# Kernel optimization log

Measured on AMD Instinct MI355X. Metric: run time of the kernel, lower is better.

The kernel has to match this reference:

```python
import jax, jax.numpy as jnp
import numpy as np

N_HEADS = 16
SCALE = 8.0  # sqrt(inner_dim // n_heads) = sqrt(64), scale='inv_sqrt'


def setup_inputs() -> dict:
    key = jax.random.key(0)
    k1, k2, k3, k4 = jax.random.split(key, 4)
    b, n, d_model, inner = 8, 2048, 1024, 1024
    x = jax.random.normal(k1, (b, n, d_model), dtype=jnp.float32)
    Wqkv = jax.random.normal(k2, (3 * inner, d_model), dtype=jnp.float32) * (1.0 / np.sqrt(d_model))
    Wproj = jax.random.normal(k3, (d_model, inner), dtype=jnp.float32) * (1.0 / np.sqrt(inner))
    bproj = jax.random.normal(k4, (d_model,), dtype=jnp.float32) * 0.01
    return {"x": x, "Wqkv": Wqkv, "Wproj": Wproj, "bproj": bproj}


def reference(x, Wqkv, Wproj, bproj):
    b, n, _ = x.shape
    qkv = jnp.einsum('bnm,fm->bnf', x, Wqkv)          # [b, n, 3*inner]
    qkv = qkv.reshape(b, n, N_HEADS, -1)              # [b, n, h, 3*dh] (einops 'b n (h d)')
    dh = qkv.shape[3] // 3
    q, k, v = qkv[..., :dh], qkv[..., dh:2 * dh], qkv[..., 2 * dh:]
    # Faithful to source: q @ k.transpose(-1,-2) on [b,n,h,dh] -> scores over HEADS, [b,n,h,h]
    scores = jnp.einsum('bnhd,bngd->bnhg', q, k) / SCALE
    attn = jax.nn.softmax(scores, axis=-1)            # softmax over last head axis
    out = jnp.einsum('bnhg,bngd->bnhd', attn, v)      # [b, n, h, dh]
    out = out.reshape(b, n, -1)                       # [b, n, inner]
    return jnp.einsum('bni,mi->bnm', out, Wproj) + bproj
```

## Files before the change

### kernel.cpp

```cpp
#include <hip/hip_runtime.h>
#include <stdint.h>

typedef __bf16 bf16_t;
typedef __bf16 bf16x8 __attribute__((ext_vector_type(8)));
typedef float f32x4 __attribute__((ext_vector_type(4)));

__device__ __forceinline__ void gload_lds16(const void* g, void* l) {
  __builtin_amdgcn_global_load_lds(
      (const __attribute__((address_space(1))) uint32_t*)g,
      (__attribute__((address_space(3))) uint32_t*)l, 16, 0, 0);
}

__global__ void cast3_f32_bf16(const float* __restrict__ a, bf16_t* __restrict__ ao, int n4a,
                               const float* __restrict__ b, bf16_t* __restrict__ bo, int n4b,
                               const float* __restrict__ c, bf16_t* __restrict__ co, int n4c) {
  int i = blockIdx.x * blockDim.x + threadIdx.x;
  int stride = gridDim.x * blockDim.x;
  int total = n4a + n4b + n4c;
  for (int idx = i; idx < total; idx += stride) {
    const float* src; bf16_t* dst; int j = idx;
    if (j < n4a) { src = a; dst = ao; }
    else if ((j -= n4a) < n4b) { src = b; dst = bo; }
    else { j -= n4b; src = c; dst = co; }
    float4 v = reinterpret_cast<const float4*>(src)[j];
    union { bf16_t b[4]; uint2 u; } pk;
    pk.b[0] = (bf16_t)v.x; pk.b[1] = (bf16_t)v.y;
    pk.b[2] = (bf16_t)v.z; pk.b[3] = (bf16_t)v.w;
    reinterpret_cast<uint2*>(dst)[j] = pk.u;
  }
}

template <bool BF16_OUT>
__global__ __launch_bounds__(512, 2)
void gemm_rp(const bf16_t* __restrict__ A, const bf16_t* __restrict__ B,
             void* __restrict__ Cout, const float* __restrict__ bias, int N) {
  constexpr int K = 1024, NT = 32;
  __shared__ bf16_t Al[4][256 * 32];
  __shared__ bf16_t Bl[4][256 * 32];

  const int tid = threadIdx.x;
  const int l = tid & 63, w = tid >> 6;
  const int wm = w >> 2, wn = w & 3;

  const int bid = blockIdx.x;
  const int xcd = bid & 7, idx = bid >> 3;
  const int bx = xcd * 8 + (idx & 7);
  const int by = idx >> 3;
  const int m0 = bx * 256, n0 = by * 256;

  const int ra = tid >> 2;
  const int ca = ((tid & 3) ^ ((tid >> 3) & 3)) * 8;
  const bf16_t* pA0 = A + (size_t)(m0 + ra) * K + ca;
  const bf16_t* pA1 = A + (size_t)(m0 + 128 + ra) * K + ca;
  const bf16_t* pB0 = B + (size_t)(n0 + ra) * K + ca;
  const bf16_t* pB1 = B + (size_t)(n0 + 128 + ra) * K + ca;
  const int wb = w * 512;

#define STAGE(t_, s_) do { const int kt_ = (t_) * 32;  \
    gload_lds16(pA0 + kt_, &Al[s_][wb]);               \
    gload_lds16(pA1 + kt_, &Al[s_][4096 + wb]);        \
    gload_lds16(pB0 + kt_, &Bl[s_][wb]);               \
    gload_lds16(pB1 + kt_, &Bl[s_][4096 + wb]); } while (0)

  const int abase = (wm * 128 + (l & 15)) * 32;
  const int bbase = (wn * 64 + (l & 15)) * 32;
  const int ck = ((l >> 4) ^ ((l >> 1) & 3)) * 8;

  f32x4 acc[8][4] = {};
  bf16x8 afA[4], bfA[4], afB[4], bfB[4], ah[4];

#define RD_LO(af_, bf_, s_) do {                                               \
    const bf16_t* As_ = Al[s_]; const bf16_t* Bs_ = Bl[s_];                    \
    _Pragma("unroll") for (int j = 0; j < 4; ++j)                              \
      bf_[j] = *reinterpret_cast<const bf16x8*>(&Bs_[bbase + j * 512 + ck]);   \
    _Pragma("unroll") for (int i = 0; i < 4; ++i)                              \
      af_[i] = *reinterpret_cast<const bf16x8*>(&As_[abase + i * 512 + ck]);   \
  } while (0)
#define RD_HI(s_) do { const bf16_t* As_ = Al[s_];                             \
    _Pragma("unroll") for (int i = 0; i < 4; ++i)                              \
      ah[i] = *reinterpret_cast<const bf16x8*>(&As_[abase + (i + 4) * 512 + ck]); \
  } while (0)

#define MM16(af_, bf_, R0)                                                     \
    __builtin_amdgcn_s_setprio(1);                                             \
    _Pragma("unroll") for (int i = 0; i < 4; ++i)                              \
    _Pragma("unroll") for (int j = 0; j < 4; ++j)                              \
      acc[(R0) + i][j] = __builtin_amdgcn_mfma_f32_16x16x32_bf16(              \
          af_[i], bf_[j], acc[(R0) + i][j], 0, 0, 0);                          \
    __builtin_amdgcn_s_setprio(0);

#define BARF() do { asm volatile("" ::: "memory");  \
    __builtin_amdgcn_s_barrier();                   \
    asm volatile("" ::: "memory"); } while (0)

#define TILE(t_, AFc, BFc, AFn, BFn) do {                                 \
    RD_HI((t_) & 3);                                                      \
    if ((t_) + 3 < NT) STAGE((t_) + 3, ((t_) + 3) & 3);                   \
    asm volatile("s_waitcnt lgkmcnt(4)" ::: "memory");                    \
    MM16(AFc, BFc, 0);                                                    \
    if ((t_) + 1 < NT) {                                                  \
      RD_LO(AFn, BFn, ((t_) + 1) & 3);                                    \
      asm volatile("s_waitcnt lgkmcnt(8)" ::: "memory");                  \
    } else {                                                              \
      asm volatile("s_waitcnt lgkmcnt(0)" ::: "memory");                  \
    }                                                                     \
    MM16(ah, BFc, 4);                                                     \
    if ((t_) + 3 < NT) asm volatile("s_waitcnt vmcnt(4)" ::: "memory");   \
    else               asm volatile("s_waitcnt vmcnt(0)" ::: "memory");   \
    BARF();                                                               \
  } while (0)

  STAGE(0, 0); STAGE(1, 1); STAGE(2, 2);
  asm volatile("s_waitcnt vmcnt(4)" ::: "memory");
  BARF();
  RD_LO(afA, bfA, 0);

  for (int tt = 0; tt < NT; tt += 2) {
    TILE(tt, afA, bfA, afB, bfB);
    TILE(tt + 1, afB, bfB, afA, bfA);
  }
#undef STAGE
#undef RD_LO
#undef RD_HI
#undef MM16
#undef BARF
#undef TILE

  const int r0 = m0 + wm * 128 + (l >> 4) * 4;
  const int c0 = n0 + wn * 64 + (l & 15);
  if (BF16_OUT) {
    bf16_t* C = (bf16_t*)Cout;
#pragma unroll
    for (int i = 0; i < 8; ++i)
#pragma unroll
      for (int j = 0; j < 4; ++j)
#pragma unroll
        for (int r = 0; r < 4; ++r)
          C[(size_t)(r0 + i * 16 + r) * N + (c0 + j * 16)] = (bf16_t)acc[i][j][r];
  } else {
    float* C = (float*)Cout;
#pragma unroll
    for (int i = 0; i < 8; ++i)
#pragma unroll
      for (int j = 0; j < 4; ++j)
#pragma unroll
        for (int r = 0; r < 4; ++r)
          C[(size_t)(r0 + i * 16 + r) * N + (c0 + j * 16)] =
              acc[i][j][r] + bias[c0 + j * 16];
  }
}

__global__ __launch_bounds__(256)
void attn_heads(const bf16_t* __restrict__ qkv, bf16_t* __restrict__ out) {
  __shared__ float s[4][3072];
  const int w = threadIdx.x >> 6, l = threadIdx.x & 63;
  const size_t t = (size_t)blockIdx.x * 4 + w;
  const bf16_t* src = qkv + t * 3072;
#pragma unroll
  for (int i = 0; i < 6; ++i) {
    int f = (i * 64 + l) * 8;
    bf16x8 v = *reinterpret_cast<const bf16x8*>(&src[f]);
#pragma unroll
    for (int jj = 0; jj < 8; ++jj) s[w][f + jj] = (float)v[jj];
  }
  __syncthreads();

  const int h = l >> 2, ss = l & 3;
  float qr[16];
  const float* qb = &s[w][h * 192 + ss * 16];
#pragma unroll
  for (int d = 0; d < 16; ++d) qr[d] = qb[d];

  float sc[16];
#pragma unroll
  for (int g = 0; g < 16; ++g) {
    const float* kk = &s[w][g * 192 + 64 + ss * 16];
    float p = 0.f;
#pragma unroll
    for (int d = 0; d < 16; ++d) p += qr[d] * kk[d];
    p += __shfl_xor(p, 1);
    p += __shfl_xor(p, 2);
    sc[g] = p * 0.125f;
  }
  float m = sc[0];
#pragma unroll
  for (int g = 1; g < 16; ++g) m = fmaxf(m, sc[g]);
  float sum = 0.f;
#pragma unroll
  for (int g = 0; g < 16; ++g) { sc[g] = __expf(sc[g] - m); sum += sc[g]; }
  float inv = 1.f / sum;

  float o[16] = {};
#pragma unroll
  for (int g = 0; g < 16; ++g) {
    float a = sc[g] * inv;
    const float* vv = &s[w][g * 192 + 128 + ss * 16];
#pragma unroll
    for (int d = 0; d < 16; ++d) o[d] += a * vv[d];
  }
  union { bf16_t b[16]; uint4 u[2]; } pk;
#pragma unroll
  for (int d = 0; d < 16; ++d) pk.b[d] = (bf16_t)o[d];
  uint4* dst = reinterpret_cast<uint4*>(out + t * 1024 + h * 64 + ss * 16);
  dst[0] = pk.u[0];
  dst[1] = pk.u[1];
}

extern "C" void kernel_launch(void* const* d_in, const int* in_sizes, int n_in,
                              void* d_out, int out_size, void* d_ws, size_t ws_size,
                              hipStream_t stream) {
  const float* x     = (const float*)d_in[0];
  const float* Wqkv  = (const float*)d_in[1];
  const float* Wproj = (const float*)d_in[2];
  const float* bproj = (const float*)d_in[3];
  float* out = (float*)d_out;

  const int M = 8 * 2048;
  const int DM = 1024;
  const int F = 3072;

  char* ws = (char*)d_ws;
  bf16_t* xb     = (bf16_t*)ws;  ws += (size_t)M * DM * 2;
  bf16_t* wqkvb  = (bf16_t*)ws;  ws += (size_t)F * DM * 2;
  bf16_t* wprojb = (bf16_t*)ws;  ws += (size_t)DM * DM * 2;
  bf16_t* qkvb   = (bf16_t*)ws;  ws += (size_t)M * F * 2;
  bf16_t* attnb  = (bf16_t*)ws;

  cast3_f32_bf16<<<2048, 256, 0, stream>>>(x, xb, M * DM / 4,
                                           Wqkv, wqkvb, F * DM / 4,
                                           Wproj, wprojb, DM * DM / 4);

  gemm_rp<true><<<(M / 256) * (F / 256), 512, 0, stream>>>(
      xb, wqkvb, (void*)qkvb, nullptr, F);

  attn_heads<<<M / 4, 256, 0, stream>>>(qkvb, attnb);

  gemm_rp<false><<<(M / 256) * (DM / 256), 512, 0, stream>>>(
      attnb, wprojb, (void*)out, bproj, DM);
}
```

Baseline: 216.2 us.

## Rewrite GEMM with 4 fat waves using 32x32x16 MFMA tiles

Restructures both GEMMs from 8 waves of 16x16x32 MFMAs into 4 waves that each own a 128x128 output tile and issue 32x32x16 bf16 MFMAs. Staging now issues eight LDS-direct loads per thread, the LDS reads use a new swizzle, and the pipeline prefetches the next tile's fragments during the current MMA. The goal is fewer LDS reads per FLOP and fewer instructions per output. In exchange there are fewer waves per CU to hide latency, a simpler wait and barrier schedule, and much higher register pressure (256 accumulator floats per thread).

```diff
diff --git a/kernel.cpp b/kernel.cpp
--- a/kernel.cpp
+++ b/kernel.cpp
@@ -3,7 +3,7 @@
 
 typedef __bf16 bf16_t;
 typedef __bf16 bf16x8 __attribute__((ext_vector_type(8)));
-typedef float f32x4 __attribute__((ext_vector_type(4)));
+typedef float f32x16 __attribute__((ext_vector_type(16)));
 
 __device__ __forceinline__ void gload_lds16(const void* g, void* l) {
   __builtin_amdgcn_global_load_lds(
@@ -31,16 +31,16 @@
 }
 
 template <bool BF16_OUT>
-__global__ __launch_bounds__(512, 2)
-void gemm_rp(const bf16_t* __restrict__ A, const bf16_t* __restrict__ B,
-             void* __restrict__ Cout, const float* __restrict__ bias, int N) {
+__global__ __launch_bounds__(256, 1)
+void gemm_fat(const bf16_t* __restrict__ A, const bf16_t* __restrict__ B,
+              void* __restrict__ Cout, const float* __restrict__ bias, int N) {
   constexpr int K = 1024, NT = 32;
   __shared__ bf16_t Al[4][256 * 32];
   __shared__ bf16_t Bl[4][256 * 32];
 
   const int tid = threadIdx.x;
   const int l = tid & 63, w = tid >> 6;
-  const int wm = w >> 2, wn = w & 3;
+  const int wm = w >> 1, wn = w & 1;
 
   const int bid = blockIdx.x;
   const int xcd = bid & 7, idx = bid >> 3;
@@ -50,103 +50,108 @@
 
   const int ra = tid >> 2;
   const int ca = ((tid & 3) ^ ((tid >> 3) & 3)) * 8;
-  const bf16_t* pA0 = A + (size_t)(m0 + ra) * K + ca;
-  const bf16_t* pA1 = A + (size_t)(m0 + 128 + ra) * K + ca;
-  const bf16_t* pB0 = B + (size_t)(n0 + ra) * K + ca;
-  const bf16_t* pB1 = B + (size_t)(n0 + 128 + ra) * K + ca;
-  const int wb = w * 512;
-
-#define STAGE(t_, s_) do { const int kt_ = (t_) * 32;  \
-    gload_lds16(pA0 + kt_, &Al[s_][wb]);               \
-    gload_lds16(pA1 + kt_, &Al[s_][4096 + wb]);        \
-    gload_lds16(pB0 + kt_, &Bl[s_][wb]);               \
-    gload_lds16(pB1 + kt_, &Bl[s_][4096 + wb]); } while (0)
-
-  const int abase = (wm * 128 + (l & 15)) * 32;
-  const int bbase = (wn * 64 + (l & 15)) * 32;
-  const int ck = ((l >> 4) ^ ((l >> 1) & 3)) * 8;
-
-  f32x4 acc[8][4] = {};
-  bf16x8 afA[4], bfA[4], afB[4], bfB[4], ah[4];
-
-#define RD_LO(af_, bf_, s_) do {                                               \
+  const bf16_t* pA0 = A + (size_t)(m0 +   0 + ra) * K + ca;
+  const bf16_t* pA1 = A + (size_t)(m0 +  64 + ra) * K + ca;
+  const bf16_t* pA2 = A + (size_t)(m0 + 128 + ra) * K + ca;
+  const bf16_t* pA3 = A + (size_t)(m0 + 192 + ra) * K + ca;
+  const bf16_t* pB0 = B + (size_t)(n0 +   0 + ra) * K + ca;
+  const bf16_t* pB1 = B + (size_t)(n0 +  64 + ra) * K + ca;
+  const bf16_t* pB2 = B + (size_t)(n0 + 128 + ra) * K + ca;
+  const bf16_t* pB3 = B + (size_t)(n0 + 192 + ra) * K + ca;
+  const int wb = tid * 8;
+
+#define STAGE(t_, s_) do { const int kt_ = (t_) * 32;     \
+    gload_lds16(pA0 + kt_, &Al[s_][0 * 2048 + wb]);       \
+    gload_lds16(pA1 + kt_, &Al[s_][1 * 2048 + wb]);       \
+    gload_lds16(pA2 + kt_, &Al[s_][2 * 2048 + wb]);       \
+    gload_lds16(pA3 + kt_, &Al[s_][3 * 2048 + wb]);       \
+    gload_lds16(pB0 + kt_, &Bl[s_][0 * 2048 + wb]);       \
+    gload_lds16(pB1 + kt_, &Bl[s_][1 * 2048 + wb]);       \
+    gload_lds16(pB2 + kt_, &Bl[s_][2 * 2048 + wb]);       \
+    gload_lds16(pB3 + kt_, &Bl[s_][3 * 2048 + wb]); } while (0)
+
+  const int abase = (wm * 128 + (l & 31)) * 32;
+  const int bbase = (wn * 128 + (l & 31)) * 32;
+  const int ck0 = (((l >> 5) + 0) ^ ((l >> 1) & 3)) * 8;
+  const int ck1 = (((l >> 5) + 2) ^ ((l >> 1) & 3)) * 8;
+
+#define RD(af_, bf_, s_) do {                                                  \
     const bf16_t* As_ = Al[s_]; const bf16_t* Bs_ = Bl[s_];                    \
-    _Pragma("unroll") for (int j = 0; j < 4; ++j)                              \
-      bf_[j] = *reinterpret_cast<const bf16x8*>(&Bs_[bbase + j * 512 + ck]);   \
-    _Pragma("unroll") for (int i = 0; i < 4; ++i)                              \
-      af_[i] = *reinterpret_cast<const bf16x8*>(&As_[abase + i * 512 + ck]);   \
-  } while (0)
-#define RD_HI(s_) do { const bf16_t* As_ = Al[s_];                             \
-    _Pragma("unroll") for (int i = 0; i < 4; ++i)                              \
-      ah[i] = *reinterpret_cast<const bf16x8*>(&As_[abase + (i + 4) * 512 + ck]); \
-  } while (0)
-
-#define MM16(af_, bf_, R0)                                                     \
+    _Pragma("unroll") for (int fr = 0; fr < 4; ++fr) {                         \
+      af_[fr][0] = *reinterpret_cast<const bf16x8*>(&As_[abase + fr * 1024 + ck0]); \
+      af_[fr][1] = *reinterpret_cast<const bf16x8*>(&As_[abase + fr * 1024 + ck1]); \
+    }                                                                          \
+    _Pragma("unroll") for (int fc = 0; fc < 4; ++fc) {                         \
+      bf_[fc][0] = *reinterpret_cast<const bf16x8*>(&Bs_[bbase + fc * 1024 + ck0]); \
+      bf_[fc][1] = *reinterpret_cast<const bf16x8*>(&Bs_[bbase + fc * 1024 + ck1]); \
+    } } while (0)
+
+#define MM32(af_, bf_)                                                         \
     __builtin_amdgcn_s_setprio(1);                                             \
-    _Pragma("unroll") for (int i = 0; i < 4; ++i)                              \
-    _Pragma("unroll") for (int j = 0; j < 4; ++j)                              \
-      acc[(R0) + i][j] = __builtin_amdgcn_mfma_f32_16x16x32_bf16(              \
-          af_[i], bf_[j], acc[(R0) + i][j], 0, 0, 0);                          \
+    _Pragma("unroll") for (int ks = 0; ks < 2; ++ks)                           \
+    _Pragma("unroll") for (int fr = 0; fr < 4; ++fr)                           \
+    _Pragma("unroll") for (int fc = 0; fc < 4; ++fc)                           \
+      acc[fr][fc] = __builtin_amdgcn_mfma_f32_32x32x16_bf16(                   \
+          af_[fr][ks], bf_[fc][ks], acc[fr][fc], 0, 0, 0);                     \
     __builtin_amdgcn_s_setprio(0);
 
 #define BARF() do { asm volatile("" ::: "memory");  \
     __builtin_amdgcn_s_barrier();                   \
     asm volatile("" ::: "memory"); } while (0)
 
-#define TILE(t_, AFc, BFc, AFn, BFn) do {                                 \
-    RD_HI((t_) & 3);                                                      \
-    if ((t_) + 3 < NT) STAGE((t_) + 3, ((t_) + 3) & 3);                   \
-    asm volatile("s_waitcnt lgkmcnt(4)" ::: "memory");                    \
-    MM16(AFc, BFc, 0);                                                    \
-    if ((t_) + 1 < NT) {                                                  \
-      RD_LO(AFn, BFn, ((t_) + 1) & 3);                                    \
-      asm volatile("s_waitcnt lgkmcnt(8)" ::: "memory");                  \
-    } else {                                                              \
-      asm volatile("s_waitcnt lgkmcnt(0)" ::: "memory");                  \
-    }                                                                     \
-    MM16(ah, BFc, 4);                                                     \
-    if ((t_) + 3 < NT) asm volatile("s_waitcnt vmcnt(4)" ::: "memory");   \
-    else               asm volatile("s_waitcnt vmcnt(0)" ::: "memory");   \
-    BARF();                                                               \
+#define TILE(t_, CA, CB, NA, NB) do {                                      \
+    if ((t_) + 3 < NT) STAGE((t_) + 3, ((t_) + 3) & 3);                    \
+    if ((t_) + 1 < NT) RD(NA, NB, ((t_) + 1) & 3);                         \
+    MM32(CA, CB);                                                          \
+    asm volatile("s_waitcnt lgkmcnt(0)" ::: "memory");                     \
+    if ((t_) < NT - 3)       asm volatile("s_waitcnt vmcnt(8)" ::: "memory"); \
+    else if ((t_) == NT - 3) asm volatile("s_waitcnt vmcnt(0)" ::: "memory"); \
+    BARF();                                                                \
   } while (0)
 
+  f32x16 acc[4][4] = {};
+  bf16x8 afA[4][2], bfA[4][2], afB[4][2], bfB[4][2];
+
   STAGE(0, 0); STAGE(1, 1); STAGE(2, 2);
-  asm volatile("s_waitcnt vmcnt(4)" ::: "memory");
+  asm volatile("s_waitcnt vmcnt(8)" ::: "memory");
   BARF();
-  RD_LO(afA, bfA, 0);
+  RD(afA, bfA, 0);
 
   for (int tt = 0; tt < NT; tt += 2) {
     TILE(tt, afA, bfA, afB, bfB);
     TILE(tt + 1, afB, bfB, afA, bfA);
   }
 #undef STAGE
-#undef RD_LO
-#undef RD_HI
-#undef MM16
+#undef RD
+#undef MM32
 #undef BARF
 #undef TILE
 
-  const int r0 = m0 + wm * 128 + (l >> 4) * 4;
-  const int c0 = n0 + wn * 64 + (l & 15);
+  const int rbase = m0 + wm * 128 + 4 * (l >> 5);
+  const int cbase = n0 + wn * 128 + (l & 31);
   if (BF16_OUT) {
     bf16_t* C = (bf16_t*)Cout;
 #pragma unroll
-    for (int i = 0; i < 8; ++i)
-#pragma unroll
-      for (int j = 0; j < 4; ++j)
-#pragma unroll
-        for (int r = 0; r < 4; ++r)
-          C[(size_t)(r0 + i * 16 + r) * N + (c0 + j * 16)] = (bf16_t)acc[i][j][r];
+    for (int fr = 0; fr < 4; ++fr)
+#pragma unroll
+      for (int fc = 0; fc < 4; ++fc)
+#pragma unroll
+        for (int rg = 0; rg < 16; ++rg) {
+          int row = rbase + fr * 32 + (rg & 3) + 8 * (rg >> 2);
+          C[(size_t)row * N + (cbase + fc * 32)] = (bf16_t)acc[fr][fc][rg];
+        }
   } else {
     float* C = (float*)Cout;
 #pragma unroll
-    for (int i = 0; i < 8; ++i)
-#pragma unroll
-      for (int j = 0; j < 4; ++j)
-#pragma unroll
-        for (int r = 0; r < 4; ++r)
-          C[(size_t)(r0 + i * 16 + r) * N + (c0 + j * 16)] =
-              acc[i][j][r] + bias[c0 + j * 16];
+    for (int fr = 0; fr < 4; ++fr)
+#pragma unroll
+      for (int fc = 0; fc < 4; ++fc)
+#pragma unroll
+        for (int rg = 0; rg < 16; ++rg) {
+          int row = rbase + fr * 32 + (rg & 3) + 8 * (rg >> 2);
+          int col = cbase + fc * 32;
+          C[(size_t)row * N + col] = acc[fr][fc][rg] + bias[col];
+        }
   }
 }
 
@@ -230,11 +235,11 @@
                                            Wqkv, wqkvb, F * DM / 4,
                                            Wproj, wprojb, DM * DM / 4);
 
-  gemm_rp<true><<<(M / 256) * (F / 256), 512, 0, stream>>>(
+  gemm_fat<true><<<(M / 256) * (F / 256), 256, 0, stream>>>(
       xb, wqkvb, (void*)qkvb, nullptr, F);
 
   attn_heads<<<M / 4, 256, 0, stream>>>(qkvb, attnb);
 
-  gemm_rp<false><<<(M / 256) * (DM / 256), 512, 0, stream>>>(
+  gemm_fat<false><<<(M / 256) * (DM / 256), 256, 0, stream>>>(
       attnb, wprojb, (void*)out, bproj, DM);
 }
```

Result: slower. 493.3 us (+128.2%).

## Rework GEMM into 4-wave 128x128 warp tiles with 3-stage LDS pipeline

Applied to the files above, without the earlier changes.

The GEMM now uses 256 threads per block instead of 512, so each wave computes a 128x128 sub-tile (8x8 MFMA accumulators) rather than 128x64. This raises register-level reuse of the A and B fragments. The 4-stage ring with split lo/hi fragment reads is replaced by a simpler 3-stage ring: each tile does a full fragment read and 64 MFMAs between two barriers. The cost is heavy register pressure (256 accumulator floats plus double-buffered fragments), occupancy limited to one block, and less fine-grained overlap of LDS reads with MFMA work.

```diff
diff --git a/kernel.cpp b/kernel.cpp
--- a/kernel.cpp
+++ b/kernel.cpp
@@ -31,16 +31,16 @@
 }
 
 template <bool BF16_OUT>
-__global__ __launch_bounds__(512, 2)
-void gemm_rp(const bf16_t* __restrict__ A, const bf16_t* __restrict__ B,
+__global__ __launch_bounds__(256, 1)
+void gemm_fw(const bf16_t* __restrict__ A, const bf16_t* __restrict__ B,
              void* __restrict__ Cout, const float* __restrict__ bias, int N) {
   constexpr int K = 1024, NT = 32;
-  __shared__ bf16_t Al[4][256 * 32];
-  __shared__ bf16_t Bl[4][256 * 32];
+  __shared__ bf16_t Al[3][256 * 32];
+  __shared__ bf16_t Bl[3][256 * 32];
 
   const int tid = threadIdx.x;
   const int l = tid & 63, w = tid >> 6;
-  const int wm = w >> 2, wn = w & 3;
+  const int wm = w >> 1, wn = w & 1;
 
   const int bid = blockIdx.x;
   const int xcd = bid & 7, idx = bid >> 3;
@@ -50,90 +50,88 @@
 
   const int ra = tid >> 2;
   const int ca = ((tid & 3) ^ ((tid >> 3) & 3)) * 8;
-  const bf16_t* pA0 = A + (size_t)(m0 + ra) * K + ca;
-  const bf16_t* pA1 = A + (size_t)(m0 + 128 + ra) * K + ca;
-  const bf16_t* pB0 = B + (size_t)(n0 + ra) * K + ca;
-  const bf16_t* pB1 = B + (size_t)(n0 + 128 + ra) * K + ca;
-  const int wb = w * 512;
-
-#define STAGE(t_, s_) do { const int kt_ = (t_) * 32;  \
-    gload_lds16(pA0 + kt_, &Al[s_][wb]);               \
-    gload_lds16(pA1 + kt_, &Al[s_][4096 + wb]);        \
-    gload_lds16(pB0 + kt_, &Bl[s_][wb]);               \
-    gload_lds16(pB1 + kt_, &Bl[s_][4096 + wb]); } while (0)
+  const bf16_t* pA = A + (size_t)(m0 + ra) * K + ca;
+  const bf16_t* pB = B + (size_t)(n0 + ra) * K + ca;
+
+#define STAGE(t_, s_) do { const int kt_ = (t_) * 32;                  \
+    gload_lds16(pA + kt_,                 &Al[s_][tid * 8]);           \
+    gload_lds16(pA + (size_t)64 * K + kt_,  &Al[s_][2048 + tid * 8]);  \
+    gload_lds16(pA + (size_t)128 * K + kt_, &Al[s_][4096 + tid * 8]);  \
+    gload_lds16(pA + (size_t)192 * K + kt_, &Al[s_][6144 + tid * 8]);  \
+    gload_lds16(pB + kt_,                 &Bl[s_][tid * 8]);           \
+    gload_lds16(pB + (size_t)64 * K + kt_,  &Bl[s_][2048 + tid * 8]);  \
+    gload_lds16(pB + (size_t)128 * K + kt_, &Bl[s_][4096 + tid * 8]);  \
+    gload_lds16(pB + (size_t)192 * K + kt_, &Bl[s_][6144 + tid * 8]);  \
+  } while (0)
 
   const int abase = (wm * 128 + (l & 15)) * 32;
-  const int bbase = (wn * 64 + (l & 15)) * 32;
+  const int bbase = (wn * 128 + (l & 15)) * 32;
   const int ck = ((l >> 4) ^ ((l >> 1) & 3)) * 8;
 
-  f32x4 acc[8][4] = {};
-  bf16x8 afA[4], bfA[4], afB[4], bfB[4], ah[4];
-
-#define RD_LO(af_, bf_, s_) do {                                               \
-    const bf16_t* As_ = Al[s_]; const bf16_t* Bs_ = Bl[s_];                    \
-    _Pragma("unroll") for (int j = 0; j < 4; ++j)                              \
-      bf_[j] = *reinterpret_cast<const bf16x8*>(&Bs_[bbase + j * 512 + ck]);   \
-    _Pragma("unroll") for (int i = 0; i < 4; ++i)                              \
-      af_[i] = *reinterpret_cast<const bf16x8*>(&As_[abase + i * 512 + ck]);   \
+#define RD(af_, bf_, s_) do {                                                 \
+    const bf16_t* As_ = Al[s_]; const bf16_t* Bs_ = Bl[s_];                   \
+    _Pragma("unroll") for (int i = 0; i < 8; ++i)                             \
+      af_[i] = *reinterpret_cast<const bf16x8*>(&As_[abase + i * 512 + ck]);  \
+    _Pragma("unroll") for (int j = 0; j < 8; ++j)                             \
+      bf_[j] = *reinterpret_cast<const bf16x8*>(&Bs_[bbase + j * 512 + ck]);  \
   } while (0)
-#define RD_HI(s_) do { const bf16_t* As_ = Al[s_];                             \
-    _Pragma("unroll") for (int i = 0; i < 4; ++i)                              \
-      ah[i] = *reinterpret_cast<const bf16x8*>(&As_[abase + (i + 4) * 512 + ck]); \
-  } while (0)
-
-#define MM16(af_, bf_, R0)                                                     \
-    __builtin_amdgcn_s_setprio(1);                                             \
-    _Pragma("unroll") for (int i = 0; i < 4; ++i)                              \
-    _Pragma("unroll") for (int j = 0; j < 4; ++j)                              \
-      acc[(R0) + i][j] = __builtin_amdgcn_mfma_f32_16x16x32_bf16(              \
-          af_[i], bf_[j], acc[(R0) + i][j], 0, 0, 0);                          \
-    __builtin_amdgcn_s_setprio(0);
+
+#define MM64(af_, bf_)                                                        \
+    _Pragma("unroll") for (int i = 0; i < 8; ++i)                             \
+    _Pragma("unroll") for (int j = 0; j < 8; ++j)                             \
+      acc[i][j] = __builtin_amdgcn_mfma_f32_16x16x32_bf16(                    \
+          af_[i], bf_[j], acc[i][j], 0, 0, 0);
 
 #define BARF() do { asm volatile("" ::: "memory");  \
     __builtin_amdgcn_s_barrier();                   \
     asm volatile("" ::: "memory"); } while (0)
 
-#define TILE(t_, AFc, BFc, AFn, BFn) do {                                 \
-    RD_HI((t_) & 3);                                                      \
-    if ((t_) + 3 < NT) STAGE((t_) + 3, ((t_) + 3) & 3);                   \
-    asm volatile("s_waitcnt lgkmcnt(4)" ::: "memory");                    \
-    MM16(AFc, BFc, 0);                                                    \
-    if ((t_) + 1 < NT) {                                                  \
-      RD_LO(AFn, BFn, ((t_) + 1) & 3);                                    \
-      asm volatile("s_waitcnt lgkmcnt(8)" ::: "memory");                  \
-    } else {                                                              \
-      asm volatile("s_waitcnt lgkmcnt(0)" ::: "memory");                  \
-    }                                                                     \
-    MM16(ah, BFc, 4);                                                     \
-    if ((t_) + 3 < NT) asm volatile("s_waitcnt vmcnt(4)" ::: "memory");   \
-    else               asm volatile("s_waitcnt vmcnt(0)" ::: "memory");   \
-    BARF();                                                               \
+#define TILE(t_, sl_, CA, CB, NA, NB) do {                                 \
+    if ((t_) + 2 < NT) {                                                   \
+      int st_ = (sl_) + 2; if (st_ >= 3) st_ -= 3;                         \
+      STAGE((t_) + 2, st_);                                                \
+      asm volatile("s_waitcnt vmcnt(8)" ::: "memory");                     \
+    } else if ((t_) + 1 < NT) {                                            \
+      asm volatile("s_waitcnt vmcnt(0)" ::: "memory");                     \
+    }                                                                      \
+    BARF();                                                                \
+    if ((t_) + 1 < NT) {                                                   \
+      int rd_ = (sl_) + 1; if (rd_ >= 3) rd_ -= 3;                         \
+      RD(NA, NB, rd_);                                                     \
+    }                                                                      \
+    MM64(CA, CB);                                                          \
+    BARF();                                                                \
   } while (0)
 
-  STAGE(0, 0); STAGE(1, 1); STAGE(2, 2);
-  asm volatile("s_waitcnt vmcnt(4)" ::: "memory");
+  f32x4 acc[8][8] = {};
+  bf16x8 afA[8], bfA[8], afB[8], bfB[8];
+
+  STAGE(0, 0); STAGE(1, 1);
+  asm volatile("s_waitcnt vmcnt(8)" ::: "memory");
   BARF();
-  RD_LO(afA, bfA, 0);
-
+  RD(afA, bfA, 0);
+
+  int sl = 0;
   for (int tt = 0; tt < NT; tt += 2) {
-    TILE(tt, afA, bfA, afB, bfB);
-    TILE(tt + 1, afB, bfB, afA, bfA);
+    TILE(tt, sl, afA, bfA, afB, bfB);
+    sl = (sl == 2) ? 0 : sl + 1;
+    TILE(tt + 1, sl, afB, bfB, afA, bfA);
+    sl = (sl == 2) ? 0 : sl + 1;
   }
 #undef STAGE
-#undef RD_LO
-#undef RD_HI
-#undef MM16
+#undef RD
+#undef MM64
 #undef BARF
 #undef TILE
 
   const int r0 = m0 + wm * 128 + (l >> 4) * 4;
-  const int c0 = n0 + wn * 64 + (l & 15);
+  const int c0 = n0 + wn * 128 + (l & 15);
   if (BF16_OUT) {
     bf16_t* C = (bf16_t*)Cout;
 #pragma unroll
     for (int i = 0; i < 8; ++i)
 #pragma unroll
-      for (int j = 0; j < 4; ++j)
+      for (int j = 0; j < 8; ++j)
 #pragma unroll
         for (int r = 0; r < 4; ++r)
           C[(size_t)(r0 + i * 16 + r) * N + (c0 + j * 16)] = (bf16_t)acc[i][j][r];
@@ -142,7 +140,7 @@
 #pragma unroll
     for (int i = 0; i < 8; ++i)
 #pragma unroll
-      for (int j = 0; j < 4; ++j)
+      for (int j = 0; j < 8; ++j)
 #pragma unroll
         for (int r = 0; r < 4; ++r)
           C[(size_t)(r0 + i * 16 + r) * N + (c0 + j * 16)] =
@@ -230,11 +228,11 @@
                                            Wqkv, wqkvb, F * DM / 4,
                                            Wproj, wprojb, DM * DM / 4);
 
-  gemm_rp<true><<<(M / 256) * (F / 256), 512, 0, stream>>>(
+  gemm_fw<true><<<(M / 256) * (F / 256), 256, 0, stream>>>(
       xb, wqkvb, (void*)qkvb, nullptr, F);
 
   attn_heads<<<M / 4, 256, 0, stream>>>(qkvb, attnb);
 
-  gemm_rp<false><<<(M / 256) * (DM / 256), 512, 0, stream>>>(
+  gemm_fw<false><<<(M / 256) * (DM / 256), 256, 0, stream>>>(
       attnb, wprojb, (void*)out, bproj, DM);
 }
```

Measured after the change: 420.2 us. 1.94x slower.

## Restructure GEMM main loop into full-tile ping-pong register prefetch with sched barrier

Applied to the files above, without the earlier changes.

The GEMM inner loop changes from a split half-tile LDS read scheme (low and high A fragments interleaved with two 16-MFMA groups and fine lgkmcnt waits) to reading the whole next tile's A and B fragments into a second register set before issuing all 32 MFMAs for the current tile. A sched_barrier pins the LDS reads and global staging ahead of the MFMA block, and the setprio hints are removed. The intent is a simpler software pipeline that hides LDS latency behind a full tile of matrix work. In exchange it holds more fragment registers at once (two 8+4 sets), which may raise register pressure under the 512x2 launch bound. Relying on the compiler rather than explicit lgkmcnt waits may also serialise the LDS reads against the MFMAs.

```diff
diff --git a/kernel.cpp b/kernel.cpp
--- a/kernel.cpp
+++ b/kernel.cpp
@@ -32,8 +32,8 @@
 
 template <bool BF16_OUT>
 __global__ __launch_bounds__(512, 2)
-void gemm_rp(const bf16_t* __restrict__ A, const bf16_t* __restrict__ B,
-             void* __restrict__ Cout, const float* __restrict__ bias, int N) {
+void gemm_pin(const bf16_t* __restrict__ A, const bf16_t* __restrict__ B,
+              void* __restrict__ Cout, const float* __restrict__ bias, int N) {
   constexpr int K = 1024, NT = 32;
   __shared__ bf16_t Al[4][256 * 32];
   __shared__ bf16_t Bl[4][256 * 32];
@@ -66,63 +66,51 @@
   const int bbase = (wn * 64 + (l & 15)) * 32;
   const int ck = ((l >> 4) ^ ((l >> 1) & 3)) * 8;
 
-  f32x4 acc[8][4] = {};
-  bf16x8 afA[4], bfA[4], afB[4], bfB[4], ah[4];
-
-#define RD_LO(af_, bf_, s_) do {                                               \
+#define RD(af_, bf_, s_) do {                                                  \
     const bf16_t* As_ = Al[s_]; const bf16_t* Bs_ = Bl[s_];                    \
+    _Pragma("unroll") for (int i = 0; i < 8; ++i)                              \
+      af_[i] = *reinterpret_cast<const bf16x8*>(&As_[abase + i * 512 + ck]);   \
     _Pragma("unroll") for (int j = 0; j < 4; ++j)                              \
       bf_[j] = *reinterpret_cast<const bf16x8*>(&Bs_[bbase + j * 512 + ck]);   \
-    _Pragma("unroll") for (int i = 0; i < 4; ++i)                              \
-      af_[i] = *reinterpret_cast<const bf16x8*>(&As_[abase + i * 512 + ck]);   \
   } while (0)
-#define RD_HI(s_) do { const bf16_t* As_ = Al[s_];                             \
-    _Pragma("unroll") for (int i = 0; i < 4; ++i)                              \
-      ah[i] = *reinterpret_cast<const bf16x8*>(&As_[abase + (i + 4) * 512 + ck]); \
-  } while (0)
-
-#define MM16(af_, bf_, R0)                                                     \
-    __builtin_amdgcn_s_setprio(1);                                             \
-    _Pragma("unroll") for (int i = 0; i < 4; ++i)                              \
+
+#define MM32(af_, bf_)                                                         \
+    _Pragma("unroll") for (int i = 0; i < 8; ++i)                              \
     _Pragma("unroll") for (int j = 0; j < 4; ++j)                              \
-      acc[(R0) + i][j] = __builtin_amdgcn_mfma_f32_16x16x32_bf16(              \
-          af_[i], bf_[j], acc[(R0) + i][j], 0, 0, 0);                          \
-    __builtin_amdgcn_s_setprio(0);
+      acc[i][j] = __builtin_amdgcn_mfma_f32_16x16x32_bf16(                     \
+          af_[i], bf_[j], acc[i][j], 0, 0, 0);
 
 #define BARF() do { asm volatile("" ::: "memory");  \
     __builtin_amdgcn_s_barrier();                   \
     asm volatile("" ::: "memory"); } while (0)
 
-#define TILE(t_, AFc, BFc, AFn, BFn) do {                                 \
-    RD_HI((t_) & 3);                                                      \
-    if ((t_) + 3 < NT) STAGE((t_) + 3, ((t_) + 3) & 3);                   \
-    asm volatile("s_waitcnt lgkmcnt(4)" ::: "memory");                    \
-    MM16(AFc, BFc, 0);                                                    \
-    if ((t_) + 1 < NT) {                                                  \
-      RD_LO(AFn, BFn, ((t_) + 1) & 3);                                    \
-      asm volatile("s_waitcnt lgkmcnt(8)" ::: "memory");                  \
-    } else {                                                              \
-      asm volatile("s_waitcnt lgkmcnt(0)" ::: "memory");                  \
-    }                                                                     \
-    MM16(ah, BFc, 4);                                                     \
-    if ((t_) + 3 < NT) asm volatile("s_waitcnt vmcnt(4)" ::: "memory");   \
-    else               asm volatile("s_waitcnt vmcnt(0)" ::: "memory");   \
-    BARF();                                                               \
+#define TILE(t_, CA, CB, NA, NB) do {                                      \
+    if ((t_) + 1 < NT) RD(NA, NB, ((t_) + 1) & 3);                         \
+    if ((t_) + 3 < NT) STAGE((t_) + 3, ((t_) + 3) & 3);                    \
+    __builtin_amdgcn_sched_barrier(0);    \
+    MM32(CA, CB);                                                          \
+    if ((t_) + 4 < NT)      asm volatile("s_waitcnt vmcnt(4)" ::: "memory"); \
+    else if ((t_) + 3 == NT - 1 + 1 - 1 && false) {}                       \
+    else if ((t_) == NT - 3) asm volatile("s_waitcnt vmcnt(0)" ::: "memory"); \
+    else if ((t_) < NT - 3)  asm volatile("s_waitcnt vmcnt(4)" ::: "memory"); \
+    BARF();                                                                \
   } while (0)
+
+  f32x4 acc[8][4] = {};
+  bf16x8 afA[8], bfA[4], afB[8], bfB[4];
 
   STAGE(0, 0); STAGE(1, 1); STAGE(2, 2);
   asm volatile("s_waitcnt vmcnt(4)" ::: "memory");
   BARF();
-  RD_LO(afA, bfA, 0);
+  RD(afA, bfA, 0);
 
   for (int tt = 0; tt < NT; tt += 2) {
     TILE(tt, afA, bfA, afB, bfB);
     TILE(tt + 1, afB, bfB, afA, bfA);
   }
 #undef STAGE
-#undef RD_LO
-#undef RD_HI
-#undef MM16
+#undef RD
+#undef MM32
 #undef BARF
 #undef TILE
 
@@ -230,11 +218,11 @@
                                            Wqkv, wqkvb, F * DM / 4,
                                            Wproj, wprojb, DM * DM / 4);
 
-  gemm_rp<true><<<(M / 256) * (F / 256), 512, 0, stream>>>(
+  gemm_pin<true><<<(M / 256) * (F / 256), 512, 0, stream>>>(
       xb, wqkvb, (void*)qkvb, nullptr, F);
 
   attn_heads<<<M / 4, 256, 0, stream>>>(qkvb, attnb);
 
-  gemm_rp<false><<<(M / 256) * (DM / 256), 512, 0, stream>>>(
+  gemm_pin<false><<<(M / 256) * (DM / 256), 512, 0, stream>>>(
       attnb, wprojb, (void*)out, bproj, DM);
 }
```

New measurement: 205.6 us. 4.9% less time.
